# Kernel tuning notes

Hardware: AMD Instinct MI355X
Metric: run time of the kernel (lower is better)

Reference implementation:

```python
import jax, jax.numpy as jnp
import numpy as np

B, S, HID, NH, HD = 2, 2048, 1024, 16, 64
SCALE = 1.0 / np.sqrt(HD)
NEG = -1e9


def _rope_cache(seq_len, dim, base=10000.0):
    inv_freq = 1.0 / (base ** (np.arange(0, dim, 2, dtype=np.float32) / dim))
    t = np.arange(seq_len, dtype=np.float32)
    freqs = np.outer(t, inv_freq)                      # [S, dim/2]
    emb = np.concatenate([freqs, freqs], axis=-1)      # [S, dim]
    return jnp.asarray(np.cos(emb)), jnp.asarray(np.sin(emb))


def _rotate_half(x):
    x1, x2 = jnp.split(x, 2, axis=-1)
    return jnp.concatenate([-x2, x1], axis=-1)


def setup_inputs() -> dict:
    key = jax.random.key(0)
    k0, k1, k2, k3, k4 = jax.random.split(key, 5)
    hidden_states = jax.random.normal(k0, (B, S, HID), jnp.float32)
    Wq = jax.random.normal(k1, (HID, NH * HD), jnp.float32) * 0.02
    Wk = jax.random.normal(k2, (HID, NH * HD), jnp.float32) * 0.02
    Wv = jax.random.normal(k3, (HID, NH * HD), jnp.float32) * 0.02
    Wo = jax.random.normal(k4, (NH * HD, HID), jnp.float32) * 0.02
    causal = jnp.tril(jnp.ones((S, S), bool))
    attention_mask = jnp.broadcast_to(
        jnp.where(causal, 0.0, NEG).astype(jnp.float32)[None, None], (B, 1, S, S))
    position_ids = jnp.broadcast_to(jnp.arange(S, dtype=jnp.int32)[None], (B, S))
    cos, sin = _rope_cache(S, HD)
    return {"hidden_states": hidden_states, "attention_mask": attention_mask,
            "position_ids": position_ids, "cos": cos, "sin": sin,
            "Wq": Wq, "Wk": Wk, "Wv": Wv, "Wo": Wo}


def reference(hidden_states, attention_mask, position_ids, cos, sin, Wq, Wk, Wv, Wo):
    b, s, _ = hidden_states.shape
    def proj(W):  # [B,S,HID] @ [HID,NH*HD] -> [B,NH,S,HD]
        return jnp.einsum('bsh,hd->bsd', hidden_states, W).reshape(b, s, NH, HD).transpose(0, 2, 1, 3)
    q, k, v = proj(Wq), proj(Wk), proj(Wv)
    # RoPE: gather per-position cos/sin -> [B,1,S,HD]
    cos_g = cos[position_ids][:, None]
    sin_g = sin[position_ids][:, None]
    q = q * cos_g + _rotate_half(q) * sin_g
    k = k * cos_g + _rotate_half(k) * sin_g
    scores = jnp.einsum('bhqd,bhkd->bhqk', q, k) * SCALE + attention_mask
    attn = jax.nn.softmax(scores.astype(jnp.float32), axis=-1).astype(q.dtype)
    out = jnp.einsum('bhqk,bhkd->bhqd', attn, v)
    out = out.transpose(0, 2, 1, 3).reshape(b, s, NH * HD)
    return jnp.einsum('bsd,dh->bsh', out, Wo)
```

## Files before the change

### kernel.cpp

```cpp
#include <hip/hip_runtime.h>

typedef __bf16 bf16x8 __attribute__((ext_vector_type(8)));
typedef float  f32x4  __attribute__((ext_vector_type(4)));
typedef unsigned short ushortx8 __attribute__((ext_vector_type(8)));
typedef unsigned short ushortx4 __attribute__((ext_vector_type(4)));

static __device__ __forceinline__ unsigned short f2bf(float f) {
  unsigned int u = __builtin_bit_cast(unsigned int, f);
  u += 0x7FFFu + ((u >> 16) & 1u);
  return (unsigned short)(u >> 16);
}
static __device__ __forceinline__ unsigned short f2bf_fast(float f) {
  unsigned int u = __builtin_bit_cast(unsigned int, f);
  return (unsigned short)((u + 0x8000u) >> 16);
}

#define GLL16(gp, lp) __builtin_amdgcn_global_load_lds(                       \
    (const __attribute__((address_space(1))) void*)(gp),                      \
    (__attribute__((address_space(3))) void*)(lp), 16, 0, 0)

__global__ __launch_bounds__(256) void prep_kernel(const float* __restrict__ X,
                                                   const float* __restrict__ W0,
                                                   const float* __restrict__ W1,
                                                   const float* __restrict__ W2,
                                                   const float* __restrict__ W3,
                                                   unsigned short* __restrict__ Xbf,
                                                   unsigned short* __restrict__ D0,
                                                   unsigned short* __restrict__ D1,
                                                   unsigned short* __restrict__ D2,
                                                   unsigned short* __restrict__ D3) {
  int z = blockIdx.z;
  if (z >= 4) {
    long bid = (long)(z - 4) * 1024 + blockIdx.y * 32 + blockIdx.x;
    int tl = threadIdx.y * 32 + threadIdx.x;
    long i = bid * 2048 + (long)tl * 8;
    float4 f0 = *(const float4*)(X + i);
    float4 f1 = *(const float4*)(X + i + 4);
    ushortx8 u;
    u[0] = f2bf(f0.x); u[1] = f2bf(f0.y); u[2] = f2bf(f0.z); u[3] = f2bf(f0.w);
    u[4] = f2bf(f1.x); u[5] = f2bf(f1.y); u[6] = f2bf(f1.z); u[7] = f2bf(f1.w);
    *(ushortx8*)(Xbf + i) = u;
    return;
  }
  const float* src = (z == 0) ? W0 : (z == 1) ? W1 : (z == 2) ? W2 : W3;
  unsigned short* dst = (z == 0) ? D0 : (z == 1) ? D1 : (z == 2) ? D2 : D3;
  const int R = 1024, C = 1024;
  __shared__ unsigned short t[32][33];
  int c = blockIdx.x * 32 + threadIdx.x;
#pragma unroll
  for (int i = 0; i < 4; ++i) {
    int r = blockIdx.y * 32 + threadIdx.y + i * 8;
    t[threadIdx.y + i * 8][threadIdx.x] = f2bf(src[(size_t)r * C + c]);
  }
  __syncthreads();
  int rr = blockIdx.y * 32 + threadIdx.x;
#pragma unroll
  for (int i = 0; i < 4; ++i) {
    int cc = blockIdx.x * 32 + threadIdx.y + i * 8;
    dst[(size_t)cc * R + rr] = t[threadIdx.x][threadIdx.y + i * 8];
  }
}

__global__ __launch_bounds__(256) void gemm128_kernel(
    const unsigned short* __restrict__ A,
    const unsigned short* __restrict__ BT0,
    const unsigned short* __restrict__ BT1,
    const unsigned short* __restrict__ BT2,
    unsigned short* __restrict__ outQ,
    unsigned short* __restrict__ outK,
    unsigned short* __restrict__ outVT,
    const int* __restrict__ pos_ids,
    const float* __restrict__ cosb,
    const float* __restrict__ sinb) {
  const int K = 1024;
  int id = blockIdx.x + 8 * (blockIdx.y + 32 * blockIdx.z);
  int m_idx = id & 31;
  int nzi = id >> 5;
  int n_idx = nzi & 7;
  int z = nzi >> 3;
  const unsigned short* BT = (z == 0) ? BT0 : (z == 1 ? BT1 : BT2);
  int n0 = n_idx * 128, m0 = m_idx * 128;
  int t = threadIdx.x, lane = t & 63, w = t >> 6;
  int wy = w >> 1, wx = w & 1;
  int n16 = lane & 15, quad = lane >> 4;
  __shared__ __align__(16) unsigned short sA0[128 * 32];
  __shared__ __align__(16) unsigned short sA1[128 * 32];
  __shared__ __align__(16) unsigned short sB0[128 * 32];
  __shared__ __align__(16) unsigned short sB1[128 * 32];

  int r4 = lane >> 2, c4 = lane & 3;
  const char* gA = (const char*)(A + (size_t)(m0 + w * 32 + r4) * K) + ((c4 ^ (r4 & 3)) * 16);
  const char* gB = (const char*)(BT + (size_t)(n0 + w * 32 + r4) * K) + ((c4 ^ (r4 & 3)) * 16);
  const size_t row16 = (size_t)16 * K * 2;

  f32x4 acc[4][4];
#pragma unroll
  for (int i = 0; i < 4; ++i)
#pragma unroll
    for (int j = 0; j < 4; ++j) acc[i][j] = f32x4{0.f, 0.f, 0.f, 0.f};

#define GSTAGE(kk_, SA, SB)                                                     \
  do {                                                                          \
    GLL16(gA + (size_t)(kk_) * 2, SA + (w * 32) * 32);                          \
    GLL16(gA + (size_t)(kk_) * 2 + row16, SA + (w * 32 + 16) * 32);             \
    GLL16(gB + (size_t)(kk_) * 2, SB + (w * 32) * 32);                          \
    GLL16(gB + (size_t)(kk_) * 2 + row16, SB + (w * 32 + 16) * 32);             \
  } while (0)

#define GCOMPUTE(SA, SB)                                                        \
  do {                                                                          \
    bf16x8 a[4], b[4];                                                          \
    int cs = (quad ^ (n16 & 3)) * 8;                                            \
    _Pragma("unroll") for (int i = 0; i < 4; ++i) {                             \
      a[i] = *(const bf16x8*)(&SA[(wy * 64 + i * 16 + n16) * 32 + cs]);         \
      b[i] = *(const bf16x8*)(&SB[(wx * 64 + i * 16 + n16) * 32 + cs]);         \
    }                                                                           \
    _Pragma("unroll") for (int mt = 0; mt < 4; ++mt)                            \
      _Pragma("unroll") for (int nt = 0; nt < 4; ++nt)                          \
        acc[mt][nt] = __builtin_amdgcn_mfma_f32_16x16x32_bf16(                  \
            a[mt], b[nt], acc[mt][nt], 0, 0, 0);                                \
  } while (0)

  GSTAGE(0, sA0, sB0);
  for (int kk = 0; kk < K;) {
    __syncthreads();
    if (kk + 32 < K) GSTAGE(kk + 32, sA1, sB1);
    GCOMPUTE(sA0, sB0);
    kk += 32;
    if (kk >= K) break;
    __syncthreads();
    if (kk + 32 < K) GSTAGE(kk + 32, sA0, sB0);
    GCOMPUTE(sA1, sB1);
    kk += 32;
  }
#undef GSTAGE
#undef GCOMPUTE

  if (z < 2) {
    const float qs = (z == 0) ? (0.125f * 1.44269504088896340736f) : 1.0f;
#pragma unroll
    for (int mt = 0; mt < 4; ++mt)
#pragma unroll
      for (int r = 0; r < 4; ++r) {
        int row = m0 + wy * 64 + mt * 16 + quad * 4 + r;
        int b = row >> 11, s = row & 2047;
        int pos = pos_ids[b * 2048 + s];
        const float* cb = cosb + (size_t)pos * 64;
        const float* sb = sinb + (size_t)pos * 64;
#pragma unroll
        for (int nt = 0; nt < 2; ++nt) {
          int d0 = nt * 16 + n16;
          float c0 = cb[d0] * qs, s0 = sb[d0] * qs;
          float c1 = cb[d0 + 32] * qs, s1 = sb[d0 + 32] * qs;
          float x0 = acc[mt][nt][r], x1 = acc[mt][nt + 2][r];
          acc[mt][nt][r]     = x0 * c0 - x1 * s0;
          acc[mt][nt + 2][r] = x1 * c1 + x0 * s1;
        }
      }
  }

  if (z == 2) {
#pragma unroll
    for (int mt = 0; mt < 4; ++mt)
#pragma unroll
      for (int nt = 0; nt < 4; ++nt) {
        int row = m0 + wy * 64 + mt * 16 + quad * 4;
        int b = row >> 11, s = row & 2047;
        int col = n0 + wx * 64 + nt * 16 + n16;
        int h = col >> 6, d = col & 63;
        ushortx4 u;
#pragma unroll
        for (int r = 0; r < 4; ++r) u[r] = f2bf(acc[mt][nt][r]);
        *(ushortx4*)(&outVT[(((size_t)b * 16 + h) * 64 + d) * 2048 + s]) = u;
      }
    return;
  }

#pragma unroll
  for (int mt = 0; mt < 4; ++mt)
#pragma unroll
    for (int nt = 0; nt < 4; ++nt)
#pragma unroll
      for (int r = 0; r < 4; ++r) {
        int row = m0 + wy * 64 + mt * 16 + quad * 4 + r;
        int col = n0 + wx * 64 + nt * 16 + n16;
        unsigned short* dst = (z == 0) ? outQ : outK;
        int b = row >> 11, s = row & 2047, h = col >> 6, d = col & 63;
        dst[(((size_t)b * 16 + h) * 2048 + s) * 64 + d] = f2bf(acc[mt][nt][r]);
      }
}

__global__ __launch_bounds__(256) void gemm64_kernel(const unsigned short* __restrict__ A,
                                                     const unsigned short* __restrict__ BT,
                                                     float* __restrict__ outF) {
  const int K = 1024, N = 1024;
  int m0 = blockIdx.x * 64, n0 = blockIdx.y * 64;
  int t = threadIdx.x, lane = t & 63, w = t >> 6;
  int wy = w >> 1, wx = w & 1;
  int n16 = lane & 15, quad = lane >> 4;
  __shared__ __align__(16) unsigned short sA0[64 * 32];
  __shared__ __align__(16) unsigned short sA1[64 * 32];
  __shared__ __align__(16) unsigned short sB0[64 * 32];
  __shared__ __align__(16) unsigned short sB1[64 * 32];

  int r4 = lane >> 2, c4 = lane & 3;
  const char* gA = (const char*)(A + (size_t)(m0 + w * 16 + r4) * K) + ((c4 ^ (r4 & 3)) * 16);
  const char* gB = (const char*)(BT + (size_t)(n0 + w * 16 + r4) * K) + ((c4 ^ (r4 & 3)) * 16);

  f32x4 acc[2][2];
#pragma unroll
  for (int i = 0; i < 2; ++i)
#pragma unroll
    for (int j = 0; j < 2; ++j) acc[i][j] = f32x4{0.f, 0.f, 0.f, 0.f};

#define WSTAGE(kk_, SA, SB)                                                     \
  do {                                                                          \
    GLL16(gA + (size_t)(kk_) * 2, SA + (w * 16) * 32);                          \
    GLL16(gB + (size_t)(kk_) * 2, SB + (w * 16) * 32);                          \
  } while (0)

#define WCOMPUTE(SA, SB)                                                        \
  do {                                                                          \
    int cs = (quad ^ (n16 & 3)) * 8;                                            \
    bf16x8 a0 = *(const bf16x8*)(&SA[(wy * 32 + n16) * 32 + cs]);               \
    bf16x8 a1 = *(const bf16x8*)(&SA[(wy * 32 + 16 + n16) * 32 + cs]);          \
    bf16x8 b0 = *(const bf16x8*)(&SB[(wx * 32 + n16) * 32 + cs]);               \
    bf16x8 b1 = *(const bf16x8*)(&SB[(wx * 32 + 16 + n16) * 32 + cs]);          \
    acc[0][0] = __builtin_amdgcn_mfma_f32_16x16x32_bf16(a0, b0, acc[0][0], 0, 0, 0); \
    acc[0][1] = __builtin_amdgcn_mfma_f32_16x16x32_bf16(a0, b1, acc[0][1], 0, 0, 0); \
    acc[1][0] = __builtin_amdgcn_mfma_f32_16x16x32_bf16(a1, b0, acc[1][0], 0, 0, 0); \
    acc[1][1] = __builtin_amdgcn_mfma_f32_16x16x32_bf16(a1, b1, acc[1][1], 0, 0, 0); \
  } while (0)

  WSTAGE(0, sA0, sB0);
  for (int kk = 0; kk < K;) {
    __syncthreads();
    if (kk + 32 < K) WSTAGE(kk + 32, sA1, sB1);
    WCOMPUTE(sA0, sB0);
    kk += 32;
    if (kk >= K) break;
    __syncthreads();
    if (kk + 32 < K) WSTAGE(kk + 32, sA0, sB0);
    WCOMPUTE(sA1, sB1);
    kk += 32;
  }
#undef WSTAGE
#undef WCOMPUTE

#pragma unroll
  for (int mt = 0; mt < 2; ++mt)
#pragma unroll
    for (int nt = 0; nt < 2; ++nt)
#pragma unroll
      for (int r = 0; r < 4; ++r) {
        int row = m0 + wy * 32 + mt * 16 + quad * 4 + r;
        int col = n0 + wx * 32 + nt * 16 + n16;
        outF[(size_t)row * N + col] = acc[mt][nt][r];
      }
}

__global__ __launch_bounds__(512) void attn_kernel(const unsigned short* __restrict__ Q,
                                                   const unsigned short* __restrict__ Kk,
                                                   const unsigned short* __restrict__ VT,
                                                   unsigned short* __restrict__ O) {
  int bh = blockIdx.x;
  int qt = (int)(gridDim.y - 1 - blockIdx.y);
  int t = threadIdx.x;
  int lane = t & 63;
  int w = t >> 6;
  int g = w >> 2;
  int w4 = w & 3;
  int n16 = lane & 15, quad = lane >> 4;
  int r8 = lane >> 3, c8 = lane & 7;
  const unsigned short* Qb = Q + (size_t)bh * 2048 * 64;
  const unsigned short* Kb = Kk + (size_t)bh * 2048 * 64;
  const unsigned short* Vb = VT + (size_t)bh * 64 * 2048;

  __shared__ __align__(16) unsigned short sKV[2 * 2 * 2 * 4096];
  __shared__ __align__(16) unsigned short sP[8][16 * 64];
  unsigned short* spW = sP[w];
  unsigned short* gBase = sKV + g * 16384;

  int b_ = bh >> 4, h_ = bh & 15;
  int nk = qt + 1;
  int u = (nk + 1) >> 1;
  int beg = g ? u : 0;
  int end = g ? nk : u;
  int qg = qt * 64 + w4 * 16 + n16;

  bf16x8 aQ[2];
#pragma unroll
  for (int kb = 0; kb < 2; ++kb)
    aQ[kb] = *(const bf16x8*)(Qb + (size_t)qg * 64 + kb * 32 + quad * 8);

  f32x4 o[4];
  float mst = -3e38f, lst = 0.f;
#pragma unroll
  for (int ct = 0; ct < 4; ++ct) o[ct] = f32x4{0.f, 0.f, 0.f, 0.f};

#define ASTAGE(kt_, BUF)                                                                  \
  do {                                                                                    \
    const unsigned short* kg_ = Kb + (size_t)((kt_) * 64 + w4 * 16) * 64;                 \
    const unsigned short* vg_ = Vb + (size_t)(w4 * 16) * 2048 + (kt_) * 64;               \
    unsigned short* dK = gBase + (BUF) * 8192 + (w4 * 16) * 64;                           \
    unsigned short* dV = dK + 4096;                                                       \
    GLL16(kg_ + (size_t)r8 * 64 + (c8 ^ r8) * 8, dK);                                     \
    GLL16(kg_ + (size_t)(8 + r8) * 64 + (c8 ^ r8) * 8, dK + 8 * 64);                      \
    GLL16(vg_ + (size_t)r8 * 2048 + (c8 ^ r8) * 8, dV);                                   \
    GLL16(vg_ + (size_t)(8 + r8) * 2048 + (c8 ^ r8) * 8, dV + 8 * 64);                    \
  } while (0)

#define ACOMPUTE(kt_, BUF)                                                                \
  do {                                                                                    \
    const unsigned short* kT_ = gBase + (BUF) * 8192;                                     \
    const unsigned short* vT_ = kT_ + 4096;                                               \
    f32x4 sc[4];                                \
    _Pragma("unroll") for (int mt = 0; mt < 4; ++mt) {                                    \
      const unsigned short* kr = &kT_[(mt * 16 + n16) * 64];                              \
      bf16x8 ka0 = *(const bf16x8*)(kr + ((quad ^ (n16 & 7)) * 8));                       \
      bf16x8 ka1 = *(const bf16x8*)(kr + (((4 + quad) ^ (n16 & 7)) * 8));                 \
      f32x4 zv = f32x4{0.f, 0.f, 0.f, 0.f};                                               \
      zv = __builtin_amdgcn_mfma_f32_16x16x32_bf16(ka0, aQ[0], zv, 0, 0, 0);              \
      sc[mt] = __builtin_amdgcn_mfma_f32_16x16x32_bf16(ka1, aQ[1], zv, 0, 0, 0);          \
    }                                                                                     \
    float p[4][4];                                                                        \
    _Pragma("unroll") for (int mt = 0; mt < 4; ++mt)                                      \
      _Pragma("unroll") for (int r = 0; r < 4; ++r) p[mt][r] = sc[mt][r];                 \
    if ((kt_) == nk - 1) {                                 \
      int kb0 = (kt_) * 64 + quad * 4;                                                    \
      _Pragma("unroll") for (int mt = 0; mt < 4; ++mt)                                    \
        _Pragma("unroll") for (int r = 0; r < 4; ++r)                                     \
          if (kb0 + mt * 16 + r > qg) p[mt][r] = -3e38f;                                  \
    }                                                                                     \
    float rm = p[0][0];                                                                   \
    _Pragma("unroll") for (int mt = 0; mt < 4; ++mt)                                      \
      _Pragma("unroll") for (int r = 0; r < 4; ++r) rm = fmaxf(rm, p[mt][r]);             \
    rm = fmaxf(rm, __shfl_xor(rm, 16));                                                   \
    rm = fmaxf(rm, __shfl_xor(rm, 32));                                                   \
    float mn = fmaxf(mst, rm);                                                            \
    float al = exp2f(mst - mn);                                                           \
    mst = mn;                                                                             \
    float rs = 0.f;                                                                       \
    _Pragma("unroll") for (int mt = 0; mt < 4; ++mt)                                      \
      _Pragma("unroll") for (int r = 0; r < 4; ++r) {                                     \
        p[mt][r] = exp2f(p[mt][r] - mn);                                                  \
        rs += p[mt][r];                                                                   \
      }                                                                                   \
    lst = lst * al + rs;                                                                  \
    _Pragma("unroll") for (int ct = 0; ct < 4; ++ct)                                      \
      _Pragma("unroll") for (int r = 0; r < 4; ++r) o[ct][r] *= al;                       \
    _Pragma("unroll") for (int mt = 0; mt < 4; ++mt) {                                    \
      ushortx4 uu;                                                                        \
      _Pragma("unroll") for (int r = 0; r < 4; ++r) uu[r] = f2bf_fast(p[mt][r]);          \
      int ch = (mt * 2 + (quad >> 1)) ^ (n16 & 7);                                        \
      *(ushortx4*)(&spW[n16 * 64 + ch * 8 + (quad & 1) * 4]) = uu;                        \
    }                                                                                     \
    __builtin_amdgcn_s_waitcnt(0xC07F);     \
    bf16x8 aP0 = *(const bf16x8*)(&spW[n16 * 64 + ((quad ^ (n16 & 7)) * 8)]);             \
    bf16x8 aP1 = *(const bf16x8*)(&spW[n16 * 64 + (((4 + quad) ^ (n16 & 7)) * 8)]);       \
    _Pragma("unroll") for (int ct = 0; ct < 4; ++ct) {                                    \
      const unsigned short* vr = &vT_[(ct * 16 + n16) * 64];                              \
      bf16x8 va0 = *(const bf16x8*)(vr + ((quad ^ (n16 & 7)) * 8));                       \
      bf16x8 va1 = *(const bf16x8*)(vr + (((4 + quad) ^ (n16 & 7)) * 8));                 \
      o[ct] = __builtin_amdgcn_mfma_f32_16x16x32_bf16(va0, aP0, o[ct], 0, 0, 0);          \
      o[ct] = __builtin_amdgcn_mfma_f32_16x16x32_bf16(va1, aP1, o[ct], 0, 0, 0);          \
    }                                                                                     \
  } while (0)

  if (beg < end) ASTAGE(beg, 0);
  int it = 0;
  while (it < u) {
    __syncthreads();
    {
      int kt = beg + it;
      if (kt + 1 < end) ASTAGE(kt + 1, 1);
      if (kt < end) ACOMPUTE(kt, 0);
    }
    if (++it >= u) break;
    __syncthreads();
    {
      int kt = beg + it;
      if (kt + 1 < end) ASTAGE(kt + 1, 0);
      if (kt < end) ACOMPUTE(kt, 1);
    }
    ++it;
  }
#undef ASTAGE
#undef ACOMPUTE

  lst += __shfl_xor(lst, 16);
  lst += __shfl_xor(lst, 32);

  __syncthreads();
  float* scratch = (float*)sKV;
  int sidx = (w4 * 64 + lane) * 18;
  if (g == 1) {
#pragma unroll
    for (int ct = 0; ct < 4; ++ct)
#pragma unroll
      for (int r = 0; r < 4; ++r) scratch[sidx + ct * 4 + r] = o[ct][r];
    scratch[sidx + 16] = mst;
    scratch[sidx + 17] = lst;
  }
  __syncthreads();
  if (g == 0) {
    float m1 = scratch[sidx + 16], l1 = scratch[sidx + 17];
    float m = fmaxf(mst, m1);
    float a0 = exp2f(mst - m), a1 = exp2f(m1 - m);
    float inv = 1.0f / (lst * a0 + l1 * a1);
#pragma unroll
    for (int ct = 0; ct < 4; ++ct) {
      ushortx4 uo;
#pragma unroll
      for (int r = 0; r < 4; ++r) {
        float v = (o[ct][r] * a0 + scratch[sidx + ct * 4 + r] * a1) * inv;
        uo[r] = f2bf(v);
      }
      size_t addr = ((size_t)b_ * 2048 + qg) * 1024 + h_ * 64 + ct * 16 + quad * 4;
      *(ushortx4*)(&O[addr]) = uo;
    }
  }
}

extern "C" void kernel_launch(void* const* d_in, const int* in_sizes, int n_in,
                              void* d_out, int out_size, void* d_ws, size_t ws_size,
                              hipStream_t stream) {
  const float* X    = (const float*)d_in[0];
  const int*   pos  = (const int*)d_in[2];
  const float* cosb = (const float*)d_in[3];
  const float* sinb = (const float*)d_in[4];
  const float* Wq   = (const float*)d_in[5];
  const float* Wk   = (const float*)d_in[6];
  const float* Wv   = (const float*)d_in[7];
  const float* Wo   = (const float*)d_in[8];
  float* out = (float*)d_out;

  char* ws = (char*)d_ws;
  const size_t SZ_X = 4096UL * 1024 * 2;
  const size_t SZ_W = 1024UL * 1024 * 2;
  unsigned short* Xbf = (unsigned short*)(ws);
  unsigned short* WTq = (unsigned short*)(ws + SZ_X);
  unsigned short* WTk = (unsigned short*)(ws + SZ_X + SZ_W);
  unsigned short* WTv = (unsigned short*)(ws + SZ_X + 2 * SZ_W);
  unsigned short* WTo = (unsigned short*)(ws + SZ_X + 3 * SZ_W);
  unsigned short* Qbf = (unsigned short*)(ws + SZ_X + 4 * SZ_W);
  unsigned short* Kbf = (unsigned short*)(ws + 2 * SZ_X + 4 * SZ_W);
  unsigned short* VTr = (unsigned short*)(ws + 3 * SZ_X + 4 * SZ_W);
  unsigned short* Obf = (unsigned short*)(ws + 4 * SZ_X + 4 * SZ_W);

  prep_kernel<<<dim3(32, 32, 6), dim3(32, 8), 0, stream>>>(
      X, Wq, Wk, Wv, Wo, Xbf, WTq, WTk, WTv, WTo);

  gemm128_kernel<<<dim3(8, 32, 3), 256, 0, stream>>>(Xbf, WTq, WTk, WTv,
                                                     Qbf, Kbf, VTr,
                                                     pos, cosb, sinb);

  attn_kernel<<<dim3(32, 32), 512, 0, stream>>>(Qbf, Kbf, VTr, Obf);

  gemm64_kernel<<<dim3(64, 16), 256, 0, stream>>>(Obf, WTo, out);
}
```

Measured before the change: 209.9 us.

## Triple-buffer GEMM pipelines, retile output projection, add lazy softmax rescale

Both GEMM kernels move from a double-buffered loop with __syncthreads to a three-stage LDS ring. Each step waits with an explicit vmcnt and a single barrier, so loads run further ahead of the MFMAs. The output-projection GEMM is retiled from 64x64 to 128x64 blocks with a remapped block index. The attention softmax now rescales the running max and accumulators only when some row's new max exceeds the old one by more than 8 (in log2 units). This removes the per-tile exp and multiply work but lets the unnormalized values grow by up to 2^8 in bf16/fp32.

```diff
diff --git a/kernel.cpp b/kernel.cpp
--- a/kernel.cpp
+++ b/kernel.cpp
@@ -61,7 +61,7 @@
   }
 }
 
-__global__ __launch_bounds__(256) void gemm128_kernel(
+__global__ __launch_bounds__(256, 3) void qkvr_kernel(
     const unsigned short* __restrict__ A,
     const unsigned short* __restrict__ BT0,
     const unsigned short* __restrict__ BT1,
@@ -83,15 +83,22 @@
   int t = threadIdx.x, lane = t & 63, w = t >> 6;
   int wy = w >> 1, wx = w & 1;
   int n16 = lane & 15, quad = lane >> 4;
-  __shared__ __align__(16) unsigned short sA0[128 * 32];
-  __shared__ __align__(16) unsigned short sA1[128 * 32];
-  __shared__ __align__(16) unsigned short sB0[128 * 32];
-  __shared__ __align__(16) unsigned short sB1[128 * 32];
+
+  __shared__ __align__(16) unsigned short sA[3][128][32];
+  __shared__ __align__(16) unsigned short sB[3][128][32];
+  __shared__ __align__(16) unsigned short sDummy[512];
+  const int BUFE = 128 * 32;
 
   int r4 = lane >> 2, c4 = lane & 3;
   const char* gA = (const char*)(A + (size_t)(m0 + w * 32 + r4) * K) + ((c4 ^ (r4 & 3)) * 16);
   const char* gB = (const char*)(BT + (size_t)(n0 + w * 32 + r4) * K) + ((c4 ^ (r4 & 3)) * 16);
   const size_t row16 = (size_t)16 * K * 2;
+  unsigned short* stA = &sA[0][w * 32][0];
+  unsigned short* stB = &sB[0][w * 32][0];
+
+  int cs = (quad ^ (n16 & 3)) * 8;
+  const unsigned short* rdA = &sA[0][wy * 64 + n16][0] + cs;
+  const unsigned short* rdB = &sB[0][wx * 64 + n16][0] + cs;
 
   f32x4 acc[4][4];
 #pragma unroll
@@ -99,42 +106,63 @@
 #pragma unroll
     for (int j = 0; j < 4; ++j) acc[i][j] = f32x4{0.f, 0.f, 0.f, 0.f};
 
-#define GSTAGE(kk_, SA, SB)                                                     \
+  bf16x8 a[4], b[4];
+
+#define QSTG(tt, dA, dB)                                                        \
   do {                                                                          \
-    GLL16(gA + (size_t)(kk_) * 2, SA + (w * 32) * 32);                          \
-    GLL16(gA + (size_t)(kk_) * 2 + row16, SA + (w * 32 + 16) * 32);             \
-    GLL16(gB + (size_t)(kk_) * 2, SB + (w * 32) * 32);                          \
-    GLL16(gB + (size_t)(kk_) * 2 + row16, SB + (w * 32 + 16) * 32);             \
-  } while (0)
-
-#define GCOMPUTE(SA, SB)                                                        \
+    GLL16(gA + (size_t)(tt) * 64, (dA));                                        \
+    GLL16(gA + (size_t)(tt) * 64 + row16, (dA) + 16 * 32);                      \
+    GLL16(gB + (size_t)(tt) * 64, (dB));                                        \
+    GLL16(gB + (size_t)(tt) * 64 + row16, (dB) + 16 * 32);                      \
+  } while (0)
+
+#define QRD(bufi)                                                               \
   do {                                                                          \
-    bf16x8 a[4], b[4];                                                          \
-    int cs = (quad ^ (n16 & 3)) * 8;                                            \
     _Pragma("unroll") for (int i = 0; i < 4; ++i) {                             \
-      a[i] = *(const bf16x8*)(&SA[(wy * 64 + i * 16 + n16) * 32 + cs]);         \
-      b[i] = *(const bf16x8*)(&SB[(wx * 64 + i * 16 + n16) * 32 + cs]);         \
+      a[i] = *(const bf16x8*)(rdA + (bufi) * BUFE + (i * 16) * 32);             \
+      b[i] = *(const bf16x8*)(rdB + (bufi) * BUFE + (i * 16) * 32);             \
     }                                                                           \
+  } while (0)
+
+#define QMM                                                                     \
+  do {                                                                          \
     _Pragma("unroll") for (int mt = 0; mt < 4; ++mt)                            \
       _Pragma("unroll") for (int nt = 0; nt < 4; ++nt)                          \
         acc[mt][nt] = __builtin_amdgcn_mfma_f32_16x16x32_bf16(                  \
             a[mt], b[nt], acc[mt][nt], 0, 0, 0);                                \
   } while (0)
 
-  GSTAGE(0, sA0, sB0);
-  for (int kk = 0; kk < K;) {
-    __syncthreads();
-    if (kk + 32 < K) GSTAGE(kk + 32, sA1, sB1);
-    GCOMPUTE(sA0, sB0);
-    kk += 32;
-    if (kk >= K) break;
-    __syncthreads();
-    if (kk + 32 < K) GSTAGE(kk + 32, sA0, sB0);
-    GCOMPUTE(sA1, sB1);
-    kk += 32;
-  }
-#undef GSTAGE
-#undef GCOMPUTE
+  QSTG(0, stA, stB);
+  QSTG(1, stA + BUFE, stB + BUFE);
+  asm volatile("s_waitcnt vmcnt(4)" ::: "memory");
+  __builtin_amdgcn_s_barrier();
+
+#pragma unroll 3
+  for (int kt = 0; kt < 30; ++kt) {
+    int buf = kt % 3;
+    int pfb = (kt + 2) % 3;
+    QRD(buf);
+    QSTG(kt + 2, stA + pfb * BUFE, stB + pfb * BUFE);
+    QMM;
+    asm volatile("s_waitcnt vmcnt(4)" ::: "memory");
+    __builtin_amdgcn_s_barrier();
+  }
+  {
+    QRD(0);
+    QSTG(31, sDummy, sDummy);
+    QMM;
+    asm volatile("s_waitcnt vmcnt(4)" ::: "memory");
+    __builtin_amdgcn_s_barrier();
+  }
+  {
+    QRD(1);
+    QSTG(31, sDummy, sDummy);
+    QMM;
+    asm volatile("s_waitcnt vmcnt(0)" ::: "memory");
+  }
+#undef QSTG
+#undef QRD
+#undef QMM
 
   if (z < 2) {
     const float qs = (z == 0) ? (0.125f * 1.44269504088896340736f) : 1.0f;
@@ -143,8 +171,8 @@
 #pragma unroll
       for (int r = 0; r < 4; ++r) {
         int row = m0 + wy * 64 + mt * 16 + quad * 4 + r;
-        int b = row >> 11, s = row & 2047;
-        int pos = pos_ids[b * 2048 + s];
+        int b_ = row >> 11, s_ = row & 2047;
+        int pos = pos_ids[b_ * 2048 + s_];
         const float* cb = cosb + (size_t)pos * 64;
         const float* sb = sinb + (size_t)pos * 64;
 #pragma unroll
@@ -157,103 +185,133 @@
           acc[mt][nt + 2][r] = x1 * c1 + x0 * s1;
         }
       }
-  }
-
-  if (z == 2) {
+    unsigned short* dst = (z == 0) ? outQ : outK;
 #pragma unroll
     for (int mt = 0; mt < 4; ++mt)
 #pragma unroll
-      for (int nt = 0; nt < 4; ++nt) {
-        int row = m0 + wy * 64 + mt * 16 + quad * 4;
-        int b = row >> 11, s = row & 2047;
-        int col = n0 + wx * 64 + nt * 16 + n16;
-        int h = col >> 6, d = col & 63;
-        ushortx4 u;
-#pragma unroll
-        for (int r = 0; r < 4; ++r) u[r] = f2bf(acc[mt][nt][r]);
-        *(ushortx4*)(&outVT[(((size_t)b * 16 + h) * 64 + d) * 2048 + s]) = u;
-      }
+      for (int nt = 0; nt < 4; ++nt)
+#pragma unroll
+        for (int r = 0; r < 4; ++r) {
+          int row = m0 + wy * 64 + mt * 16 + quad * 4 + r;
+          int col = n0 + wx * 64 + nt * 16 + n16;
+          int b_ = row >> 11, s_ = row & 2047, h_ = col >> 6, d_ = col & 63;
+          dst[(((size_t)b_ * 16 + h_) * 2048 + s_) * 64 + d_] = f2bf(acc[mt][nt][r]);
+        }
     return;
   }
 
 #pragma unroll
   for (int mt = 0; mt < 4; ++mt)
 #pragma unroll
-    for (int nt = 0; nt < 4; ++nt)
-#pragma unroll
-      for (int r = 0; r < 4; ++r) {
-        int row = m0 + wy * 64 + mt * 16 + quad * 4 + r;
-        int col = n0 + wx * 64 + nt * 16 + n16;
-        unsigned short* dst = (z == 0) ? outQ : outK;
-        int b = row >> 11, s = row & 2047, h = col >> 6, d = col & 63;
-        dst[(((size_t)b * 16 + h) * 2048 + s) * 64 + d] = f2bf(acc[mt][nt][r]);
-      }
-}
-
-__global__ __launch_bounds__(256) void gemm64_kernel(const unsigned short* __restrict__ A,
-                                                     const unsigned short* __restrict__ BT,
-                                                     float* __restrict__ outF) {
+    for (int nt = 0; nt < 4; ++nt) {
+      int row = m0 + wy * 64 + mt * 16 + quad * 4;
+      int b_ = row >> 11, s_ = row & 2047;
+      int col = n0 + wx * 64 + nt * 16 + n16;
+      int h_ = col >> 6, d_ = col & 63;
+      ushortx4 u;
+#pragma unroll
+      for (int r = 0; r < 4; ++r) u[r] = f2bf(acc[mt][nt][r]);
+      *(ushortx4*)(&outVT[(((size_t)b_ * 16 + h_) * 64 + d_) * 2048 + s_]) = u;
+    }
+}
+
+__global__ __launch_bounds__(256) void wor_kernel(const unsigned short* __restrict__ A,
+                                                  const unsigned short* __restrict__ BT,
+                                                  float* __restrict__ outF) {
   const int K = 1024, N = 1024;
-  int m0 = blockIdx.x * 64, n0 = blockIdx.y * 64;
+  int id = blockIdx.x + 8 * blockIdx.y;
+  int m_idx = id & 31, n_idx = id >> 5;
+  int m0 = m_idx * 128, n0 = n_idx * 64;
   int t = threadIdx.x, lane = t & 63, w = t >> 6;
   int wy = w >> 1, wx = w & 1;
   int n16 = lane & 15, quad = lane >> 4;
-  __shared__ __align__(16) unsigned short sA0[64 * 32];
-  __shared__ __align__(16) unsigned short sA1[64 * 32];
-  __shared__ __align__(16) unsigned short sB0[64 * 32];
-  __shared__ __align__(16) unsigned short sB1[64 * 32];
+
+  __shared__ __align__(16) unsigned short sA[3][128][32];
+  __shared__ __align__(16) unsigned short sB[3][64][32];
+  __shared__ __align__(16) unsigned short sDummy[512];
+  const int BUFA = 128 * 32, BUFB = 64 * 32;
 
   int r4 = lane >> 2, c4 = lane & 3;
-  const char* gA = (const char*)(A + (size_t)(m0 + w * 16 + r4) * K) + ((c4 ^ (r4 & 3)) * 16);
+  const char* gA = (const char*)(A + (size_t)(m0 + w * 32 + r4) * K) + ((c4 ^ (r4 & 3)) * 16);
   const char* gB = (const char*)(BT + (size_t)(n0 + w * 16 + r4) * K) + ((c4 ^ (r4 & 3)) * 16);
-
-  f32x4 acc[2][2];
-#pragma unroll
-  for (int i = 0; i < 2; ++i)
+  const size_t row16 = (size_t)16 * K * 2;
+  unsigned short* stA = &sA[0][w * 32][0];
+  unsigned short* stB = &sB[0][w * 16][0];
+
+  int cs = (quad ^ (n16 & 3)) * 8;
+  const unsigned short* rdA = &sA[0][wy * 64 + n16][0] + cs;
+  const unsigned short* rdB = &sB[0][wx * 32 + n16][0] + cs;
+
+  f32x4 acc[4][2];
+#pragma unroll
+  for (int i = 0; i < 4; ++i)
 #pragma unroll
     for (int j = 0; j < 2; ++j) acc[i][j] = f32x4{0.f, 0.f, 0.f, 0.f};
 
-#define WSTAGE(kk_, SA, SB)                                                     \
+  bf16x8 a[4], b[2];
+
+#define WSTG(tt, dA, dB)                                                        \
   do {                                                                          \
-    GLL16(gA + (size_t)(kk_) * 2, SA + (w * 16) * 32);                          \
-    GLL16(gB + (size_t)(kk_) * 2, SB + (w * 16) * 32);                          \
-  } while (0)
-
-#define WCOMPUTE(SA, SB)                                                        \
+    GLL16(gA + (size_t)(tt) * 64, (dA));                                        \
+    GLL16(gA + (size_t)(tt) * 64 + row16, (dA) + 16 * 32);                      \
+    GLL16(gB + (size_t)(tt) * 64, (dB));                                        \
+  } while (0)
+
+#define WRD(bufi)                                                               \
   do {                                                                          \
-    int cs = (quad ^ (n16 & 3)) * 8;                                            \
-    bf16x8 a0 = *(const bf16x8*)(&SA[(wy * 32 + n16) * 32 + cs]);               \
-    bf16x8 a1 = *(const bf16x8*)(&SA[(wy * 32 + 16 + n16) * 32 + cs]);          \
-    bf16x8 b0 = *(const bf16x8*)(&SB[(wx * 32 + n16) * 32 + cs]);               \
-    bf16x8 b1 = *(const bf16x8*)(&SB[(wx * 32 + 16 + n16) * 32 + cs]);          \
-    acc[0][0] = __builtin_amdgcn_mfma_f32_16x16x32_bf16(a0, b0, acc[0][0], 0, 0, 0); \
-    acc[0][1] = __builtin_amdgcn_mfma_f32_16x16x32_bf16(a0, b1, acc[0][1], 0, 0, 0); \
-    acc[1][0] = __builtin_amdgcn_mfma_f32_16x16x32_bf16(a1, b0, acc[1][0], 0, 0, 0); \
-    acc[1][1] = __builtin_amdgcn_mfma_f32_16x16x32_bf16(a1, b1, acc[1][1], 0, 0, 0); \
-  } while (0)
-
-  WSTAGE(0, sA0, sB0);
-  for (int kk = 0; kk < K;) {
-    __syncthreads();
-    if (kk + 32 < K) WSTAGE(kk + 32, sA1, sB1);
-    WCOMPUTE(sA0, sB0);
-    kk += 32;
-    if (kk >= K) break;
-    __syncthreads();
-    if (kk + 32 < K) WSTAGE(kk + 32, sA0, sB0);
-    WCOMPUTE(sA1, sB1);
-    kk += 32;
-  }
-#undef WSTAGE
-#undef WCOMPUTE
-
-#pragma unroll
-  for (int mt = 0; mt < 2; ++mt)
+    _Pragma("unroll") for (int i = 0; i < 4; ++i)                               \
+      a[i] = *(const bf16x8*)(rdA + (bufi) * BUFA + (i * 16) * 32);             \
+    _Pragma("unroll") for (int j = 0; j < 2; ++j)                               \
+      b[j] = *(const bf16x8*)(rdB + (bufi) * BUFB + (j * 16) * 32);             \
+  } while (0)
+
+#define WMM                                                                     \
+  do {                                                                          \
+    _Pragma("unroll") for (int mt = 0; mt < 4; ++mt)                            \
+      _Pragma("unroll") for (int nt = 0; nt < 2; ++nt)                          \
+        acc[mt][nt] = __builtin_amdgcn_mfma_f32_16x16x32_bf16(                  \
+            a[mt], b[nt], acc[mt][nt], 0, 0, 0);                                \
+  } while (0)
+
+  WSTG(0, stA, stB);
+  WSTG(1, stA + BUFA, stB + BUFB);
+  asm volatile("s_waitcnt vmcnt(3)" ::: "memory");
+  __builtin_amdgcn_s_barrier();
+
+#pragma unroll 3
+  for (int kt = 0; kt < 30; ++kt) {
+    int buf = kt % 3;
+    int pfb = (kt + 2) % 3;
+    WRD(buf);
+    WSTG(kt + 2, stA + pfb * BUFA, stB + pfb * BUFB);
+    WMM;
+    asm volatile("s_waitcnt vmcnt(3)" ::: "memory");
+    __builtin_amdgcn_s_barrier();
+  }
+  {
+    WRD(0);
+    WSTG(31, sDummy, sDummy);
+    WMM;
+    asm volatile("s_waitcnt vmcnt(3)" ::: "memory");
+    __builtin_amdgcn_s_barrier();
+  }
+  {
+    WRD(1);
+    WSTG(31, sDummy, sDummy);
+    WMM;
+    asm volatile("s_waitcnt vmcnt(0)" ::: "memory");
+  }
+#undef WSTG
+#undef WRD
+#undef WMM
+
+#pragma unroll
+  for (int mt = 0; mt < 4; ++mt)
 #pragma unroll
     for (int nt = 0; nt < 2; ++nt)
 #pragma unroll
       for (int r = 0; r < 4; ++r) {
-        int row = m0 + wy * 32 + mt * 16 + quad * 4 + r;
+        int row = m0 + wy * 64 + mt * 16 + quad * 4 + r;
         int col = n0 + wx * 32 + nt * 16 + n16;
         outF[(size_t)row * N + col] = acc[mt][nt][r];
       }
@@ -337,18 +395,21 @@
       _Pragma("unroll") for (int r = 0; r < 4; ++r) rm = fmaxf(rm, p[mt][r]);             \
     rm = fmaxf(rm, __shfl_xor(rm, 16));                                                   \
     rm = fmaxf(rm, __shfl_xor(rm, 32));                                                   \
-    float mn = fmaxf(mst, rm);                                                            \
-    float al = exp2f(mst - mn);                                                           \
-    mst = mn;                                                                             \
+    if (!__all(rm <= mst + 8.f)) {        \
+      float mn = fmaxf(mst, rm);                                                          \
+      float al = exp2f(mst - mn);                                                         \
+      mst = mn;                                                                           \
+      lst *= al;                                                                          \
+      _Pragma("unroll") for (int ct = 0; ct < 4; ++ct)                                    \
+        _Pragma("unroll") for (int r = 0; r < 4; ++r) o[ct][r] *= al;                     \
+    }                                                                                     \
     float rs = 0.f;                                                                       \
     _Pragma("unroll") for (int mt = 0; mt < 4; ++mt)                                      \
       _Pragma("unroll") for (int r = 0; r < 4; ++r) {                                     \
-        p[mt][r] = exp2f(p[mt][r] - mn);                                                  \
+        p[mt][r] = exp2f(p[mt][r] - mst);                                                 \
         rs += p[mt][r];                                                                   \
       }                                                                                   \
-    lst = lst * al + rs;                                                                  \
-    _Pragma("unroll") for (int ct = 0; ct < 4; ++ct)                                      \
-      _Pragma("unroll") for (int r = 0; r < 4; ++r) o[ct][r] *= al;                       \
+    lst += rs;                                                                            \
     _Pragma("unroll") for (int mt = 0; mt < 4; ++mt) {                                    \
       ushortx4 uu;                                                                        \
       _Pragma("unroll") for (int r = 0; r < 4; ++r) uu[r] = f2bf_fast(p[mt][r]);          \
@@ -451,11 +512,11 @@
   prep_kernel<<<dim3(32, 32, 6), dim3(32, 8), 0, stream>>>(
       X, Wq, Wk, Wv, Wo, Xbf, WTq, WTk, WTv, WTo);
 
-  gemm128_kernel<<<dim3(8, 32, 3), 256, 0, stream>>>(Xbf, WTq, WTk, WTv,
-                                                     Qbf, Kbf, VTr,
-                                                     pos, cosb, sinb);
+  qkvr_kernel<<<dim3(8, 32, 3), 256, 0, stream>>>(Xbf, WTq, WTk, WTv,
+                                                  Qbf, Kbf, VTr,
+                                                  pos, cosb, sinb);
 
   attn_kernel<<<dim3(32, 32), 512, 0, stream>>>(Qbf, Kbf, VTr, Obf);
 
-  gemm64_kernel<<<dim3(64, 16), 256, 0, stream>>>(Obf, WTo, out);
-}
+  wor_kernel<<<dim3(8, 64), 256, 0, stream>>>(Obf, WTo, out);
+}
```

Result: faster. 201.7 us (-3.9%).
